# Kernel tuning notes

Hardware: AMD Instinct MI355X
Metric: run time of the kernel (lower is better)

## Reference

```python
import jax, jax.numpy as jnp
import numpy as np

SCALE = 0.125  # 1/sqrt(d_head=64)

def setup_inputs() -> dict:
    key = jax.random.key(0)
    kq, kk, kv = jax.random.split(key, 3)
    B, S, D = 16, 2048, 64
    q = jax.random.normal(kq, (B, S, D), dtype=jnp.float32)
    k = jax.random.normal(kk, (B, S, D), dtype=jnp.float32)
    v = jax.random.normal(kv, (B, S, D), dtype=jnp.float32)
    return {"q": q, "k": k, "v": v}

def reference(q, k, v):
    # scores: [B, S, S] = q @ k^T * scale
    scores = jnp.einsum('bqd,bkd->bqk', q, k) * SCALE
    attention = jax.nn.softmax(scores, axis=2)
    # dropout p=0.0 -> identity (eval); attn_mask=None -> no masking
    context = jnp.einsum('bqk,bkd->bqd', attention, v)
    return (context, attention)
```

## Files before the change

kernel.cpp:

```cpp
#include <hip/hip_runtime.h>

#define BB 16
#define SS 2048
#define DD 64
#define L2E 1.44269504f
#define A3C 4.32808512f

typedef _Float16 half8 __attribute__((ext_vector_type(8)));
typedef _Float16 half4 __attribute__((ext_vector_type(4)));
typedef float f32x4 __attribute__((ext_vector_type(4)));

typedef const __attribute__((address_space(1))) void* gas_ptr;
typedef __attribute__((address_space(3))) void* las_ptr;

#define TILE_SYNC(N)                                            \
  do {                                                          \
    asm volatile("s_waitcnt vmcnt(" #N ")" ::: "memory");       \
    __builtin_amdgcn_s_barrier();                               \
    __builtin_amdgcn_sched_barrier(0);                          \
  } while (0)

__global__ __launch_bounds__(256) void setup_kernel(const float* __restrict__ K,
                                                    const float* __restrict__ V,
                                                    _Float16* __restrict__ Kh,
                                                    _Float16* __restrict__ VT) {
  __shared__ float tile[64][65];
  int b = blockIdx.x >> 5, kt = blockIdx.x & 31;
  int tid = threadIdx.x;
  size_t base = ((size_t)b * SS + (size_t)kt * 64) * DD;
  const float4* Kq = (const float4*)(K + base);
  const float4* Vq = (const float4*)(V + base);
  half4* Khq = (half4*)(Kh + base);
#pragma unroll
  for (int it = 0; it < 4; ++it) {
    int i = tid + it * 256;
    float4 kv = Kq[i];
    half4 h;
    h[0] = (_Float16)kv.x; h[1] = (_Float16)kv.y;
    h[2] = (_Float16)kv.z; h[3] = (_Float16)kv.w;
    Khq[i] = h;
    float4 vv = Vq[i];
    int row = i >> 4, c4 = (i & 15) << 2;
    tile[row][c4 + 0] = vv.x; tile[row][c4 + 1] = vv.y;
    tile[row][c4 + 2] = vv.z; tile[row][c4 + 3] = vv.w;
  }
  __syncthreads();
  int d = tid >> 2, seg = tid & 3;
  half8 o0, o1;
#pragma unroll
  for (int j = 0; j < 8; ++j) o0[j] = (_Float16)tile[seg * 16 + j][d];
#pragma unroll
  for (int j = 0; j < 8; ++j) o1[j] = (_Float16)tile[seg * 16 + 8 + j][d];
  _Float16* dst = VT + ((size_t)b * DD + d) * SS + (size_t)kt * 64 + seg * 16;
  *(half8*)dst = o0;
  *(half8*)(dst + 8) = o1;
}

__device__ __forceinline__ void stage64(const _Float16* __restrict__ gbase, size_t rstride,
                                        _Float16* lds, int tid) {
  int w = tid >> 6, lam = tid & 63;
#pragma unroll
  for (int a = 0; a < 2; ++a) {
    int rloc = lam >> 3;
    int r = w * 16 + a * 8 + rloc;
    int byt = ((lam & 7) * 16) ^ (rloc << 4);
    const _Float16* g = gbase + (size_t)r * rstride + (byt >> 1);
    _Float16* lp = lds + (w * 16 + a * 8) * 64;
    __builtin_amdgcn_global_load_lds((gas_ptr)g, (las_ptr)lp, 16, 0, 0);
  }
}

__global__ __launch_bounds__(256, 2) void attn_kernel(const float* __restrict__ Q,
                                                      const _Float16* __restrict__ Kh,
                                                      const _Float16* __restrict__ VT,
                                                      float* __restrict__ ctx_out,
                                                      float* __restrict__ attn_out) {
  __shared__ __attribute__((aligned(16))) _Float16 Kl[2][64 * 64];
  __shared__ __attribute__((aligned(16))) _Float16 Vl[2][64 * 64];

  int tid = threadIdx.x;
  int w = tid >> 6, l = tid & 63, g = l >> 4, c = l & 15;
  int bid = (int)blockIdx.x;
  int remap = (bid & 7) * 64 + (bid >> 3);
  int b = remap >> 5, qb = remap & 31;
  size_t qrow0 = (size_t)b * SS + (size_t)qb * 64;
  size_t qr = qrow0 + (size_t)w * 16;
  const _Float16* KB = Kh + (size_t)b * SS * DD;
  const _Float16* VB = VT + (size_t)b * DD * SS;
  int swz = (c & 7) << 4;

  stage64(KB, DD, Kl[0], tid);

  half8 qa0, qa1;
  {
    const float* Qp = Q + (qr + c) * DD + 8 * g;
    float4 v0 = *(const float4*)(Qp);
    float4 v1 = *(const float4*)(Qp + 4);
    float4 v2 = *(const float4*)(Qp + 32);
    float4 v3 = *(const float4*)(Qp + 36);
    qa0[0] = (_Float16)(v0.x * 0.125f); qa0[1] = (_Float16)(v0.y * 0.125f);
    qa0[2] = (_Float16)(v0.z * 0.125f); qa0[3] = (_Float16)(v0.w * 0.125f);
    qa0[4] = (_Float16)(v1.x * 0.125f); qa0[5] = (_Float16)(v1.y * 0.125f);
    qa0[6] = (_Float16)(v1.z * 0.125f); qa0[7] = (_Float16)(v1.w * 0.125f);
    qa1[0] = (_Float16)(v2.x * 0.125f); qa1[1] = (_Float16)(v2.y * 0.125f);
    qa1[2] = (_Float16)(v2.z * 0.125f); qa1[3] = (_Float16)(v2.w * 0.125f);
    qa1[4] = (_Float16)(v3.x * 0.125f); qa1[5] = (_Float16)(v3.y * 0.125f);
    qa1[6] = (_Float16)(v3.z * 0.125f); qa1[7] = (_Float16)(v3.w * 0.125f);
  }

  TILE_SYNC(0);

  float lsum = 0.f;
  int cur = 0;
  for (int t = 0; t < 32; ++t) {
    if (t < 31) stage64(KB + (size_t)(t + 1) * 64 * DD, DD, Kl[cur ^ 1], tid);
#pragma unroll
    for (int kt = 0; kt < 4; ++kt) {
      const _Float16* kb = &Kl[cur][(kt * 16 + c) * 64];
      half8 kf0 = *(const half8*)(kb + (((16 * g) ^ swz) >> 1));
      half8 kf1 = *(const half8*)(kb + (((64 + 16 * g) ^ swz) >> 1));
      f32x4 s = {0.f, 0.f, 0.f, 0.f};
      s = __builtin_amdgcn_mfma_f32_16x16x32_f16(kf0, qa0, s, 0, 0, 0);
      s = __builtin_amdgcn_mfma_f32_16x16x32_f16(kf1, qa1, s, 0, 0, 0);
      lsum += exp2f(fmaf(s[0], L2E, -A3C)) + exp2f(fmaf(s[1], L2E, -A3C)) +
              exp2f(fmaf(s[2], L2E, -A3C)) + exp2f(fmaf(s[3], L2E, -A3C));
    }
    if (t < 31) { TILE_SYNC(0); cur ^= 1; }
  }
  lsum += __shfl_xor(lsum, 16);
  lsum += __shfl_xor(lsum, 32);
  float Ac = -__log2f(lsum) - A3C;

  __syncthreads();

  stage64(KB, DD, Kl[0], tid);
  stage64(VB, SS, Vl[0], tid);
  TILE_SYNC(0);

  f32x4 cacc[4] = {{0.f, 0.f, 0.f, 0.f}, {0.f, 0.f, 0.f, 0.f},
                   {0.f, 0.f, 0.f, 0.f}, {0.f, 0.f, 0.f, 0.f}};
  cur = 0;
  for (int t = 0; t < 32; ++t) {
    if (t < 31) {
      stage64(KB + (size_t)(t + 1) * 64 * DD, DD, Kl[cur ^ 1], tid);
      stage64(VB + (size_t)(t + 1) * 64, SS, Vl[cur ^ 1], tid);
    }
#pragma unroll
    for (int kt = 0; kt < 4; ++kt) {
      const _Float16* kb = &Kl[cur][(kt * 16 + c) * 64];
      half8 kf0 = *(const half8*)(kb + (((16 * g) ^ swz) >> 1));
      half8 kf1 = *(const half8*)(kb + (((64 + 16 * g) ^ swz) >> 1));
      f32x4 s = {0.f, 0.f, 0.f, 0.f};
      s = __builtin_amdgcn_mfma_f32_16x16x32_f16(kf0, qa0, s, 0, 0, 0);
      s = __builtin_amdgcn_mfma_f32_16x16x32_f16(kf1, qa1, s, 0, 0, 0);

      float p0 = exp2f(fmaf(s[0], L2E, Ac));
      float p1 = exp2f(fmaf(s[1], L2E, Ac));
      float p2 = exp2f(fmaf(s[2], L2E, Ac));
      float p3 = exp2f(fmaf(s[3], L2E, Ac));
      float4 st = {p0, p1, p2, p3};
      *(float4*)(attn_out + (qr + c) * SS + t * 64 + kt * 16 + 4 * g) = st;

      half4 pf;
      pf[0] = (_Float16)p0; pf[1] = (_Float16)p1;
      pf[2] = (_Float16)p2; pf[3] = (_Float16)p3;
#pragma unroll
      for (int dt = 0; dt < 4; ++dt) {
        const _Float16* vb = &Vl[cur][(dt * 16 + c) * 64];
        half4 vf = *(const half4*)(vb + (((32 * kt + 8 * g) ^ swz) >> 1));
        cacc[dt] = __builtin_amdgcn_mfma_f32_16x16x16f16(pf, vf, cacc[dt], 0, 0, 0);
      }
    }
    if (t < 31) { TILE_SYNC(4); cur ^= 1; }
  }

#pragma unroll
  for (int dt = 0; dt < 4; ++dt)
#pragma unroll
    for (int j = 0; j < 4; ++j)
      ctx_out[(qr + 4 * g + j) * DD + dt * 16 + c] = cacc[dt][j];
}

extern "C" void kernel_launch(void* const* d_in, const int* in_sizes, int n_in,
                              void* d_out, int out_size, void* d_ws, size_t ws_size,
                              hipStream_t stream) {
  const float* q = (const float*)d_in[0];
  const float* k = (const float*)d_in[1];
  const float* v = (const float*)d_in[2];
  float* ctx = (float*)d_out;
  float* attn = ctx + (size_t)BB * SS * DD;
  _Float16* Kh = (_Float16*)d_ws;
  _Float16* VT = Kh + (size_t)BB * SS * DD;
  setup_kernel<<<dim3(BB * 32), dim3(256), 0, stream>>>(k, v, Kh, VT);
  attn_kernel<<<dim3(BB * 32), dim3(256), 0, stream>>>(q, Kh, VT, ctx, attn);
}
```

Measured before the change: 103.2 us.

## Split softmax-denominator pass into its own kernel and drop LDS staging

Moves the row-sum (log-sum-exp) pass into a separate sumk kernel that splits keys across four waves, writes a per-row offset to workspace, and uses many more blocks. The main attention kernel now reads K and V^T fragments straight from global memory instead of double-buffered LDS staging with barriers. Each 16-row query slab is split across two waves by key halves, with partial contexts reduced through shared memory. The aim is more parallelism and occupancy and no per-tile barriers, at the cost of an extra launch and possibly less efficient, uncoalesced direct global fragment loads.

```diff
diff --git a/kernel.cpp b/kernel.cpp
--- a/kernel.cpp
+++ b/kernel.cpp
@@ -9,16 +9,6 @@
 typedef _Float16 half8 __attribute__((ext_vector_type(8)));
 typedef _Float16 half4 __attribute__((ext_vector_type(4)));
 typedef float f32x4 __attribute__((ext_vector_type(4)));
-
-typedef const __attribute__((address_space(1))) void* gas_ptr;
-typedef __attribute__((address_space(3))) void* las_ptr;
-
-#define TILE_SYNC(N)                                            \
-  do {                                                          \
-    asm volatile("s_waitcnt vmcnt(" #N ")" ::: "memory");       \
-    __builtin_amdgcn_s_barrier();                               \
-    __builtin_amdgcn_sched_barrier(0);                          \
-  } while (0)
 
 __global__ __launch_bounds__(256) void setup_kernel(const float* __restrict__ K,
                                                     const float* __restrict__ V,
@@ -56,129 +46,133 @@
   *(half8*)(dst + 8) = o1;
 }
 
-__device__ __forceinline__ void stage64(const _Float16* __restrict__ gbase, size_t rstride,
-                                        _Float16* lds, int tid) {
-  int w = tid >> 6, lam = tid & 63;
-#pragma unroll
-  for (int a = 0; a < 2; ++a) {
-    int rloc = lam >> 3;
-    int r = w * 16 + a * 8 + rloc;
-    int byt = ((lam & 7) * 16) ^ (rloc << 4);
-    const _Float16* g = gbase + (size_t)r * rstride + (byt >> 1);
-    _Float16* lp = lds + (w * 16 + a * 8) * 64;
-    __builtin_amdgcn_global_load_lds((gas_ptr)g, (las_ptr)lp, 16, 0, 0);
+__device__ __forceinline__ void load_qfrag(const float* __restrict__ Qp,
+                                           half8& qa0, half8& qa1) {
+  float4 v0 = *(const float4*)(Qp);
+  float4 v1 = *(const float4*)(Qp + 4);
+  float4 v2 = *(const float4*)(Qp + 32);
+  float4 v3 = *(const float4*)(Qp + 36);
+  qa0[0] = (_Float16)(v0.x * 0.125f); qa0[1] = (_Float16)(v0.y * 0.125f);
+  qa0[2] = (_Float16)(v0.z * 0.125f); qa0[3] = (_Float16)(v0.w * 0.125f);
+  qa0[4] = (_Float16)(v1.x * 0.125f); qa0[5] = (_Float16)(v1.y * 0.125f);
+  qa0[6] = (_Float16)(v1.z * 0.125f); qa0[7] = (_Float16)(v1.w * 0.125f);
+  qa1[0] = (_Float16)(v2.x * 0.125f); qa1[1] = (_Float16)(v2.y * 0.125f);
+  qa1[2] = (_Float16)(v2.z * 0.125f); qa1[3] = (_Float16)(v2.w * 0.125f);
+  qa1[4] = (_Float16)(v3.x * 0.125f); qa1[5] = (_Float16)(v3.y * 0.125f);
+  qa1[6] = (_Float16)(v3.z * 0.125f); qa1[7] = (_Float16)(v3.w * 0.125f);
+}
+
+__global__ __launch_bounds__(256, 8) void sumk_kernel(const float* __restrict__ Q,
+                                                      const _Float16* __restrict__ Kh,
+                                                      float* __restrict__ Ac) {
+  __shared__ float red[4][16];
+  int tid = threadIdx.x;
+  int w = tid >> 6, l = tid & 63, g = l >> 4, c = l & 15;
+  int bid = (int)blockIdx.x;
+  int remap = (bid & 7) * 256 + (bid >> 3);
+  int b = remap >> 7, qb = remap & 127;
+  size_t qr = (size_t)b * SS + (size_t)qb * 16;
+
+  half8 qa0, qa1;
+  load_qfrag(Q + (qr + c) * DD + 8 * g, qa0, qa1);
+
+  const _Float16* KhB = Kh + ((size_t)b * SS + w * 512 + c) * DD + 8 * g;
+  float lsum = 0.f;
+#pragma unroll 4
+  for (int t = 0; t < 32; ++t) {
+    const _Float16* kr = KhB + (size_t)t * 16 * DD;
+    half8 kf0 = *(const half8*)(kr);
+    half8 kf1 = *(const half8*)(kr + 32);
+    f32x4 s = {0.f, 0.f, 0.f, 0.f};
+    s = __builtin_amdgcn_mfma_f32_16x16x32_f16(kf0, qa0, s, 0, 0, 0);
+    s = __builtin_amdgcn_mfma_f32_16x16x32_f16(kf1, qa1, s, 0, 0, 0);
+    lsum += exp2f(fmaf(s[0], L2E, -A3C)) + exp2f(fmaf(s[1], L2E, -A3C)) +
+            exp2f(fmaf(s[2], L2E, -A3C)) + exp2f(fmaf(s[3], L2E, -A3C));
+  }
+  lsum += __shfl_xor(lsum, 16);
+  lsum += __shfl_xor(lsum, 32);
+  if (l < 16) red[w][l] = lsum;
+  __syncthreads();
+  if (tid < 16) {
+    float total = red[0][tid] + red[1][tid] + red[2][tid] + red[3][tid];
+    Ac[qr + tid] = -__log2f(total) - A3C;
   }
 }
 
-__global__ __launch_bounds__(256, 2) void attn_kernel(const float* __restrict__ Q,
+__global__ __launch_bounds__(256, 4) void attn_kernel(const float* __restrict__ Q,
                                                       const _Float16* __restrict__ Kh,
                                                       const _Float16* __restrict__ VT,
+                                                      const float* __restrict__ Ac,
                                                       float* __restrict__ ctx_out,
                                                       float* __restrict__ attn_out) {
-  __shared__ __attribute__((aligned(16))) _Float16 Kl[2][64 * 64];
-  __shared__ __attribute__((aligned(16))) _Float16 Vl[2][64 * 64];
+  __shared__ float cb[2][16][68];
 
   int tid = threadIdx.x;
   int w = tid >> 6, l = tid & 63, g = l >> 4, c = l & 15;
   int bid = (int)blockIdx.x;
-  int remap = (bid & 7) * 64 + (bid >> 3);
-  int b = remap >> 5, qb = remap & 31;
-  size_t qrow0 = (size_t)b * SS + (size_t)qb * 64;
-  size_t qr = qrow0 + (size_t)w * 16;
-  const _Float16* KB = Kh + (size_t)b * SS * DD;
-  const _Float16* VB = VT + (size_t)b * DD * SS;
-  int swz = (c & 7) << 4;
-
-  stage64(KB, DD, Kl[0], tid);
+  int remap = (bid & 7) * 128 + (bid >> 3);
+  int b = remap >> 6, qb = remap & 63;
+  size_t qr = (size_t)b * SS + (size_t)qb * 32 + (size_t)(w >> 1) * 16;
+  int k0 = (w & 1) << 10;
 
   half8 qa0, qa1;
-  {
-    const float* Qp = Q + (qr + c) * DD + 8 * g;
-    float4 v0 = *(const float4*)(Qp);
-    float4 v1 = *(const float4*)(Qp + 4);
-    float4 v2 = *(const float4*)(Qp + 32);
-    float4 v3 = *(const float4*)(Qp + 36);
-    qa0[0] = (_Float16)(v0.x * 0.125f); qa0[1] = (_Float16)(v0.y * 0.125f);
-    qa0[2] = (_Float16)(v0.z * 0.125f); qa0[3] = (_Float16)(v0.w * 0.125f);
-    qa0[4] = (_Float16)(v1.x * 0.125f); qa0[5] = (_Float16)(v1.y * 0.125f);
-    qa0[6] = (_Float16)(v1.z * 0.125f); qa0[7] = (_Float16)(v1.w * 0.125f);
-    qa1[0] = (_Float16)(v2.x * 0.125f); qa1[1] = (_Float16)(v2.y * 0.125f);
-    qa1[2] = (_Float16)(v2.z * 0.125f); qa1[3] = (_Float16)(v2.w * 0.125f);
-    qa1[4] = (_Float16)(v3.x * 0.125f); qa1[5] = (_Float16)(v3.y * 0.125f);
-    qa1[6] = (_Float16)(v3.z * 0.125f); qa1[7] = (_Float16)(v3.w * 0.125f);
-  }
+  load_qfrag(Q + (qr + c) * DD + 8 * g, qa0, qa1);
+  float ac = Ac[qr + c];
 
-  TILE_SYNC(0);
-
-  float lsum = 0.f;
-  int cur = 0;
-  for (int t = 0; t < 32; ++t) {
-    if (t < 31) stage64(KB + (size_t)(t + 1) * 64 * DD, DD, Kl[cur ^ 1], tid);
-#pragma unroll
-    for (int kt = 0; kt < 4; ++kt) {
-      const _Float16* kb = &Kl[cur][(kt * 16 + c) * 64];
-      half8 kf0 = *(const half8*)(kb + (((16 * g) ^ swz) >> 1));
-      half8 kf1 = *(const half8*)(kb + (((64 + 16 * g) ^ swz) >> 1));
-      f32x4 s = {0.f, 0.f, 0.f, 0.f};
-      s = __builtin_amdgcn_mfma_f32_16x16x32_f16(kf0, qa0, s, 0, 0, 0);
-      s = __builtin_amdgcn_mfma_f32_16x16x32_f16(kf1, qa1, s, 0, 0, 0);
-      lsum += exp2f(fmaf(s[0], L2E, -A3C)) + exp2f(fmaf(s[1], L2E, -A3C)) +
-              exp2f(fmaf(s[2], L2E, -A3C)) + exp2f(fmaf(s[3], L2E, -A3C));
-    }
-    if (t < 31) { TILE_SYNC(0); cur ^= 1; }
-  }
-  lsum += __shfl_xor(lsum, 16);
-  lsum += __shfl_xor(lsum, 32);
-  float Ac = -__log2f(lsum) - A3C;
-
-  __syncthreads();
-
-  stage64(KB, DD, Kl[0], tid);
-  stage64(VB, SS, Vl[0], tid);
-  TILE_SYNC(0);
+  const _Float16* KhB = Kh + ((size_t)b * SS + k0 + c) * DD + 8 * g;
+  const _Float16* VTB = VT + ((size_t)b * DD + c) * SS + k0 + 4 * g;
+  float* ap0 = attn_out + (qr + c) * SS + k0 + 4 * g;
 
   f32x4 cacc[4] = {{0.f, 0.f, 0.f, 0.f}, {0.f, 0.f, 0.f, 0.f},
                    {0.f, 0.f, 0.f, 0.f}, {0.f, 0.f, 0.f, 0.f}};
-  cur = 0;
-  for (int t = 0; t < 32; ++t) {
-    if (t < 31) {
-      stage64(KB + (size_t)(t + 1) * 64 * DD, DD, Kl[cur ^ 1], tid);
-      stage64(VB + (size_t)(t + 1) * 64, SS, Vl[cur ^ 1], tid);
-    }
-#pragma unroll
-    for (int kt = 0; kt < 4; ++kt) {
-      const _Float16* kb = &Kl[cur][(kt * 16 + c) * 64];
-      half8 kf0 = *(const half8*)(kb + (((16 * g) ^ swz) >> 1));
-      half8 kf1 = *(const half8*)(kb + (((64 + 16 * g) ^ swz) >> 1));
-      f32x4 s = {0.f, 0.f, 0.f, 0.f};
-      s = __builtin_amdgcn_mfma_f32_16x16x32_f16(kf0, qa0, s, 0, 0, 0);
-      s = __builtin_amdgcn_mfma_f32_16x16x32_f16(kf1, qa1, s, 0, 0, 0);
 
-      float p0 = exp2f(fmaf(s[0], L2E, Ac));
-      float p1 = exp2f(fmaf(s[1], L2E, Ac));
-      float p2 = exp2f(fmaf(s[2], L2E, Ac));
-      float p3 = exp2f(fmaf(s[3], L2E, Ac));
-      float4 st = {p0, p1, p2, p3};
-      *(float4*)(attn_out + (qr + c) * SS + t * 64 + kt * 16 + 4 * g) = st;
+#pragma unroll 2
+  for (int t = 0; t < 64; ++t) {
+    const _Float16* kr = KhB + (size_t)t * 16 * DD;
+    half8 kf0 = *(const half8*)(kr);
+    half8 kf1 = *(const half8*)(kr + 32);
+    half4 vf0 = *(const half4*)(VTB + t * 16);
+    half4 vf1 = *(const half4*)(VTB + 16 * SS + t * 16);
+    half4 vf2 = *(const half4*)(VTB + 32 * SS + t * 16);
+    half4 vf3 = *(const half4*)(VTB + 48 * SS + t * 16);
 
-      half4 pf;
-      pf[0] = (_Float16)p0; pf[1] = (_Float16)p1;
-      pf[2] = (_Float16)p2; pf[3] = (_Float16)p3;
-#pragma unroll
-      for (int dt = 0; dt < 4; ++dt) {
-        const _Float16* vb = &Vl[cur][(dt * 16 + c) * 64];
-        half4 vf = *(const half4*)(vb + (((32 * kt + 8 * g) ^ swz) >> 1));
-        cacc[dt] = __builtin_amdgcn_mfma_f32_16x16x16f16(pf, vf, cacc[dt], 0, 0, 0);
-      }
-    }
-    if (t < 31) { TILE_SYNC(4); cur ^= 1; }
+    f32x4 s = {0.f, 0.f, 0.f, 0.f};
+    s = __builtin_amdgcn_mfma_f32_16x16x32_f16(kf0, qa0, s, 0, 0, 0);
+    s = __builtin_amdgcn_mfma_f32_16x16x32_f16(kf1, qa1, s, 0, 0, 0);
+
+    float p0 = exp2f(fmaf(s[0], L2E, ac));
+    float p1 = exp2f(fmaf(s[1], L2E, ac));
+    float p2 = exp2f(fmaf(s[2], L2E, ac));
+    float p3 = exp2f(fmaf(s[3], L2E, ac));
+    float4 st = {p0, p1, p2, p3};
+    *(float4*)(ap0 + t * 16) = st;
+
+    half4 pf;
+    pf[0] = (_Float16)p0; pf[1] = (_Float16)p1;
+    pf[2] = (_Float16)p2; pf[3] = (_Float16)p3;
+    cacc[0] = __builtin_amdgcn_mfma_f32_16x16x16f16(pf, vf0, cacc[0], 0, 0, 0);
+    cacc[1] = __builtin_amdgcn_mfma_f32_16x16x16f16(pf, vf1, cacc[1], 0, 0, 0);
+    cacc[2] = __builtin_amdgcn_mfma_f32_16x16x16f16(pf, vf2, cacc[2], 0, 0, 0);
+    cacc[3] = __builtin_amdgcn_mfma_f32_16x16x16f16(pf, vf3, cacc[3], 0, 0, 0);
   }
 
+  int pair = w >> 1;
+  if (w & 1) {
 #pragma unroll
-  for (int dt = 0; dt < 4; ++dt)
+    for (int dt = 0; dt < 4; ++dt)
 #pragma unroll
-    for (int j = 0; j < 4; ++j)
-      ctx_out[(qr + 4 * g + j) * DD + dt * 16 + c] = cacc[dt][j];
+      for (int j = 0; j < 4; ++j)
+        cb[pair][4 * g + j][dt * 16 + c] = cacc[dt][j];
+  }
+  __syncthreads();
+  if (!(w & 1)) {
+#pragma unroll
+    for (int dt = 0; dt < 4; ++dt)
+#pragma unroll
+      for (int j = 0; j < 4; ++j)
+        ctx_out[(qr + 4 * g + j) * DD + dt * 16 + c] =
+            cacc[dt][j] + cb[pair][4 * g + j][dt * 16 + c];
+  }
 }
 
 extern "C" void kernel_launch(void* const* d_in, const int* in_sizes, int n_in,
@@ -191,6 +185,8 @@
   float* attn = ctx + (size_t)BB * SS * DD;
   _Float16* Kh = (_Float16*)d_ws;
   _Float16* VT = Kh + (size_t)BB * SS * DD;
+  float* Ac = (float*)(VT + (size_t)BB * DD * SS);
   setup_kernel<<<dim3(BB * 32), dim3(256), 0, stream>>>(k, v, Kh, VT);
-  attn_kernel<<<dim3(BB * 32), dim3(256), 0, stream>>>(q, Kh, VT, ctx, attn);
+  sumk_kernel<<<dim3(BB * 128), dim3(256), 0, stream>>>(q, Kh, Ac);
+  attn_kernel<<<dim3(BB * 64), dim3(256), 0, stream>>>(q, Kh, VT, Ac, ctx, attn);
 }
```

Result: slower. 257.8 us (+149.9%).

## Split softmax normalizer pass into a separate kernel launch

Applied to the files above, without the earlier changes.

Moves the first pass, which computes the row-wise log-sum-exp over all keys, into its own sumk_kernel that writes per-row constants to workspace. The attention kernel then reloads Q and the constant and runs only the normalize-store-PV pass. This lets the normalizer pass run without the Vl LDS allocation, and lets the two phases be scheduled as separate grids, possibly improving occupancy or overlap. The cost is an extra launch, reloading Q, and the Ac buffer round trip through memory.

```diff
diff --git a/kernel.cpp b/kernel.cpp
--- a/kernel.cpp
+++ b/kernel.cpp
@@ -70,43 +70,39 @@
   }
 }
 
-__global__ __launch_bounds__(256, 2) void attn_kernel(const float* __restrict__ Q,
+__device__ __forceinline__ void load_qfrag(const float* __restrict__ Qp,
+                                           half8& qa0, half8& qa1) {
+  float4 v0 = *(const float4*)(Qp);
+  float4 v1 = *(const float4*)(Qp + 4);
+  float4 v2 = *(const float4*)(Qp + 32);
+  float4 v3 = *(const float4*)(Qp + 36);
+  qa0[0] = (_Float16)(v0.x * 0.125f); qa0[1] = (_Float16)(v0.y * 0.125f);
+  qa0[2] = (_Float16)(v0.z * 0.125f); qa0[3] = (_Float16)(v0.w * 0.125f);
+  qa0[4] = (_Float16)(v1.x * 0.125f); qa0[5] = (_Float16)(v1.y * 0.125f);
+  qa0[6] = (_Float16)(v1.z * 0.125f); qa0[7] = (_Float16)(v1.w * 0.125f);
+  qa1[0] = (_Float16)(v2.x * 0.125f); qa1[1] = (_Float16)(v2.y * 0.125f);
+  qa1[2] = (_Float16)(v2.z * 0.125f); qa1[3] = (_Float16)(v2.w * 0.125f);
+  qa1[4] = (_Float16)(v3.x * 0.125f); qa1[5] = (_Float16)(v3.y * 0.125f);
+  qa1[6] = (_Float16)(v3.z * 0.125f); qa1[7] = (_Float16)(v3.w * 0.125f);
+}
+
+__global__ __launch_bounds__(256, 2) void sumk_kernel(const float* __restrict__ Q,
                                                       const _Float16* __restrict__ Kh,
-                                                      const _Float16* __restrict__ VT,
-                                                      float* __restrict__ ctx_out,
-                                                      float* __restrict__ attn_out) {
+                                                      float* __restrict__ Ac) {
   __shared__ __attribute__((aligned(16))) _Float16 Kl[2][64 * 64];
-  __shared__ __attribute__((aligned(16))) _Float16 Vl[2][64 * 64];
-
   int tid = threadIdx.x;
   int w = tid >> 6, l = tid & 63, g = l >> 4, c = l & 15;
   int bid = (int)blockIdx.x;
   int remap = (bid & 7) * 64 + (bid >> 3);
   int b = remap >> 5, qb = remap & 31;
-  size_t qrow0 = (size_t)b * SS + (size_t)qb * 64;
-  size_t qr = qrow0 + (size_t)w * 16;
+  size_t qr = (size_t)b * SS + (size_t)qb * 64 + (size_t)w * 16;
   const _Float16* KB = Kh + (size_t)b * SS * DD;
-  const _Float16* VB = VT + (size_t)b * DD * SS;
   int swz = (c & 7) << 4;
 
   stage64(KB, DD, Kl[0], tid);
 
   half8 qa0, qa1;
-  {
-    const float* Qp = Q + (qr + c) * DD + 8 * g;
-    float4 v0 = *(const float4*)(Qp);
-    float4 v1 = *(const float4*)(Qp + 4);
-    float4 v2 = *(const float4*)(Qp + 32);
-    float4 v3 = *(const float4*)(Qp + 36);
-    qa0[0] = (_Float16)(v0.x * 0.125f); qa0[1] = (_Float16)(v0.y * 0.125f);
-    qa0[2] = (_Float16)(v0.z * 0.125f); qa0[3] = (_Float16)(v0.w * 0.125f);
-    qa0[4] = (_Float16)(v1.x * 0.125f); qa0[5] = (_Float16)(v1.y * 0.125f);
-    qa0[6] = (_Float16)(v1.z * 0.125f); qa0[7] = (_Float16)(v1.w * 0.125f);
-    qa1[0] = (_Float16)(v2.x * 0.125f); qa1[1] = (_Float16)(v2.y * 0.125f);
-    qa1[2] = (_Float16)(v2.z * 0.125f); qa1[3] = (_Float16)(v2.w * 0.125f);
-    qa1[4] = (_Float16)(v3.x * 0.125f); qa1[5] = (_Float16)(v3.y * 0.125f);
-    qa1[6] = (_Float16)(v3.z * 0.125f); qa1[7] = (_Float16)(v3.w * 0.125f);
-  }
+  load_qfrag(Q + (qr + c) * DD + 8 * g, qa0, qa1);
 
   TILE_SYNC(0);
 
@@ -129,17 +125,40 @@
   }
   lsum += __shfl_xor(lsum, 16);
   lsum += __shfl_xor(lsum, 32);
-  float Ac = -__log2f(lsum) - A3C;
-
-  __syncthreads();
+  if (l < 16) Ac[qr + l] = -__log2f(lsum) - A3C;
+}
+
+__global__ __launch_bounds__(256, 2) void attn_kernel(const float* __restrict__ Q,
+                                                      const _Float16* __restrict__ Kh,
+                                                      const _Float16* __restrict__ VT,
+                                                      const float* __restrict__ Ac,
+                                                      float* __restrict__ ctx_out,
+                                                      float* __restrict__ attn_out) {
+  __shared__ __attribute__((aligned(16))) _Float16 Kl[2][64 * 64];
+  __shared__ __attribute__((aligned(16))) _Float16 Vl[2][64 * 64];
+
+  int tid = threadIdx.x;
+  int w = tid >> 6, l = tid & 63, g = l >> 4, c = l & 15;
+  int bid = (int)blockIdx.x;
+  int remap = (bid & 7) * 64 + (bid >> 3);
+  int b = remap >> 5, qb = remap & 31;
+  size_t qr = (size_t)b * SS + (size_t)qb * 64 + (size_t)w * 16;
+  const _Float16* KB = Kh + (size_t)b * SS * DD;
+  const _Float16* VB = VT + (size_t)b * DD * SS;
+  int swz = (c & 7) << 4;
 
   stage64(KB, DD, Kl[0], tid);
   stage64(VB, SS, Vl[0], tid);
+
+  half8 qa0, qa1;
+  load_qfrag(Q + (qr + c) * DD + 8 * g, qa0, qa1);
+  float ac = Ac[qr + c];
+
   TILE_SYNC(0);
 
   f32x4 cacc[4] = {{0.f, 0.f, 0.f, 0.f}, {0.f, 0.f, 0.f, 0.f},
                    {0.f, 0.f, 0.f, 0.f}, {0.f, 0.f, 0.f, 0.f}};
-  cur = 0;
+  int cur = 0;
   for (int t = 0; t < 32; ++t) {
     if (t < 31) {
       stage64(KB + (size_t)(t + 1) * 64 * DD, DD, Kl[cur ^ 1], tid);
@@ -154,10 +173,10 @@
       s = __builtin_amdgcn_mfma_f32_16x16x32_f16(kf0, qa0, s, 0, 0, 0);
       s = __builtin_amdgcn_mfma_f32_16x16x32_f16(kf1, qa1, s, 0, 0, 0);
 
-      float p0 = exp2f(fmaf(s[0], L2E, Ac));
-      float p1 = exp2f(fmaf(s[1], L2E, Ac));
-      float p2 = exp2f(fmaf(s[2], L2E, Ac));
-      float p3 = exp2f(fmaf(s[3], L2E, Ac));
+      float p0 = exp2f(fmaf(s[0], L2E, ac));
+      float p1 = exp2f(fmaf(s[1], L2E, ac));
+      float p2 = exp2f(fmaf(s[2], L2E, ac));
+      float p3 = exp2f(fmaf(s[3], L2E, ac));
       float4 st = {p0, p1, p2, p3};
       *(float4*)(attn_out + (qr + c) * SS + t * 64 + kt * 16 + 4 * g) = st;
 
@@ -191,6 +210,8 @@
   float* attn = ctx + (size_t)BB * SS * DD;
   _Float16* Kh = (_Float16*)d_ws;
   _Float16* VT = Kh + (size_t)BB * SS * DD;
+  float* Ac = (float*)(VT + (size_t)BB * DD * SS);
   setup_kernel<<<dim3(BB * 32), dim3(256), 0, stream>>>(k, v, Kh, VT);
-  attn_kernel<<<dim3(BB * 32), dim3(256), 0, stream>>>(q, Kh, VT, ctx, attn);
-}
+  sumk_kernel<<<dim3(BB * 32), dim3(256), 0, stream>>>(q, Kh, Ac);
+  attn_kernel<<<dim3(BB * 32), dim3(256), 0, stream>>>(q, Kh, VT, Ac, ctx, attn);
+}
```

Result: slower. 113.6 us (+10.1%).

## Triple-buffer K/V LDS tiles with prefetch distance two and single barrier

Applied to the files above, without the earlier changes.

Grows the K and V shared-memory staging from two buffers to three and prefetches tiles two iterations ahead. Each loop iteration now uses one barrier at the top, with vmcnt counts chosen so that one tile of async global->LDS loads stays in flight while the current tile is computed. This targets the load latency exposed in both passes over K/V, which are bandwidth-heavy because of the large attention-matrix stores. In exchange, shared memory per block rises to 48KB, which could limit occupancy, and the hand-computed vmcnt values are fragile because the attention stores also count against vmcnt.

```diff
diff --git a/kernel.cpp b/kernel.cpp
--- a/kernel.cpp
+++ b/kernel.cpp
@@ -70,53 +70,54 @@
   }
 }
 
+__device__ __forceinline__ void load_qfrag(const float* __restrict__ Qp,
+                                           half8& qa0, half8& qa1) {
+  float4 v0 = *(const float4*)(Qp);
+  float4 v1 = *(const float4*)(Qp + 4);
+  float4 v2 = *(const float4*)(Qp + 32);
+  float4 v3 = *(const float4*)(Qp + 36);
+  qa0[0] = (_Float16)(v0.x * 0.125f); qa0[1] = (_Float16)(v0.y * 0.125f);
+  qa0[2] = (_Float16)(v0.z * 0.125f); qa0[3] = (_Float16)(v0.w * 0.125f);
+  qa0[4] = (_Float16)(v1.x * 0.125f); qa0[5] = (_Float16)(v1.y * 0.125f);
+  qa0[6] = (_Float16)(v1.z * 0.125f); qa0[7] = (_Float16)(v1.w * 0.125f);
+  qa1[0] = (_Float16)(v2.x * 0.125f); qa1[1] = (_Float16)(v2.y * 0.125f);
+  qa1[2] = (_Float16)(v2.z * 0.125f); qa1[3] = (_Float16)(v2.w * 0.125f);
+  qa1[4] = (_Float16)(v3.x * 0.125f); qa1[5] = (_Float16)(v3.y * 0.125f);
+  qa1[6] = (_Float16)(v3.z * 0.125f); qa1[7] = (_Float16)(v3.w * 0.125f);
+}
+
 __global__ __launch_bounds__(256, 2) void attn_kernel(const float* __restrict__ Q,
                                                       const _Float16* __restrict__ Kh,
                                                       const _Float16* __restrict__ VT,
                                                       float* __restrict__ ctx_out,
                                                       float* __restrict__ attn_out) {
-  __shared__ __attribute__((aligned(16))) _Float16 Kl[2][64 * 64];
-  __shared__ __attribute__((aligned(16))) _Float16 Vl[2][64 * 64];
+  __shared__ __attribute__((aligned(16))) _Float16 Kl[3][64 * 64];
+  __shared__ __attribute__((aligned(16))) _Float16 Vl[3][64 * 64];
 
   int tid = threadIdx.x;
   int w = tid >> 6, l = tid & 63, g = l >> 4, c = l & 15;
   int bid = (int)blockIdx.x;
   int remap = (bid & 7) * 64 + (bid >> 3);
   int b = remap >> 5, qb = remap & 31;
-  size_t qrow0 = (size_t)b * SS + (size_t)qb * 64;
-  size_t qr = qrow0 + (size_t)w * 16;
+  size_t qr = (size_t)b * SS + (size_t)qb * 64 + (size_t)w * 16;
   const _Float16* KB = Kh + (size_t)b * SS * DD;
   const _Float16* VB = VT + (size_t)b * DD * SS;
   int swz = (c & 7) << 4;
 
   stage64(KB, DD, Kl[0], tid);
+  stage64(KB + (size_t)64 * DD, DD, Kl[1], tid);
 
   half8 qa0, qa1;
-  {
-    const float* Qp = Q + (qr + c) * DD + 8 * g;
-    float4 v0 = *(const float4*)(Qp);
-    float4 v1 = *(const float4*)(Qp + 4);
-    float4 v2 = *(const float4*)(Qp + 32);
-    float4 v3 = *(const float4*)(Qp + 36);
-    qa0[0] = (_Float16)(v0.x * 0.125f); qa0[1] = (_Float16)(v0.y * 0.125f);
-    qa0[2] = (_Float16)(v0.z * 0.125f); qa0[3] = (_Float16)(v0.w * 0.125f);
-    qa0[4] = (_Float16)(v1.x * 0.125f); qa0[5] = (_Float16)(v1.y * 0.125f);
-    qa0[6] = (_Float16)(v1.z * 0.125f); qa0[7] = (_Float16)(v1.w * 0.125f);
-    qa1[0] = (_Float16)(v2.x * 0.125f); qa1[1] = (_Float16)(v2.y * 0.125f);
-    qa1[2] = (_Float16)(v2.z * 0.125f); qa1[3] = (_Float16)(v2.w * 0.125f);
-    qa1[4] = (_Float16)(v3.x * 0.125f); qa1[5] = (_Float16)(v3.y * 0.125f);
-    qa1[6] = (_Float16)(v3.z * 0.125f); qa1[7] = (_Float16)(v3.w * 0.125f);
-  }
-
-  TILE_SYNC(0);
+  load_qfrag(Q + (qr + c) * DD + 8 * g, qa0, qa1);
 
   float lsum = 0.f;
-  int cur = 0;
+  int bufc = 0, bufs = 2;
   for (int t = 0; t < 32; ++t) {
-    if (t < 31) stage64(KB + (size_t)(t + 1) * 64 * DD, DD, Kl[cur ^ 1], tid);
+    if (t < 31) TILE_SYNC(2); else TILE_SYNC(0);
+    if (t + 2 < 32) stage64(KB + (size_t)(t + 2) * 64 * DD, DD, Kl[bufs], tid);
 #pragma unroll
     for (int kt = 0; kt < 4; ++kt) {
-      const _Float16* kb = &Kl[cur][(kt * 16 + c) * 64];
+      const _Float16* kb = &Kl[bufc][(kt * 16 + c) * 64];
       half8 kf0 = *(const half8*)(kb + (((16 * g) ^ swz) >> 1));
       half8 kf1 = *(const half8*)(kb + (((64 + 16 * g) ^ swz) >> 1));
       f32x4 s = {0.f, 0.f, 0.f, 0.f};
@@ -125,39 +126,45 @@
       lsum += exp2f(fmaf(s[0], L2E, -A3C)) + exp2f(fmaf(s[1], L2E, -A3C)) +
               exp2f(fmaf(s[2], L2E, -A3C)) + exp2f(fmaf(s[3], L2E, -A3C));
     }
-    if (t < 31) { TILE_SYNC(0); cur ^= 1; }
+    bufc = (bufc == 2) ? 0 : bufc + 1;
+    bufs = (bufs == 2) ? 0 : bufs + 1;
   }
   lsum += __shfl_xor(lsum, 16);
   lsum += __shfl_xor(lsum, 32);
-  float Ac = -__log2f(lsum) - A3C;
+  float ac = -__log2f(lsum) - A3C;
 
   __syncthreads();
 
   stage64(KB, DD, Kl[0], tid);
   stage64(VB, SS, Vl[0], tid);
-  TILE_SYNC(0);
+  stage64(KB + (size_t)64 * DD, DD, Kl[1], tid);
+  stage64(VB + 64, SS, Vl[1], tid);
 
   f32x4 cacc[4] = {{0.f, 0.f, 0.f, 0.f}, {0.f, 0.f, 0.f, 0.f},
                    {0.f, 0.f, 0.f, 0.f}, {0.f, 0.f, 0.f, 0.f}};
-  cur = 0;
+  bufc = 0; bufs = 2;
   for (int t = 0; t < 32; ++t) {
-    if (t < 31) {
-      stage64(KB + (size_t)(t + 1) * 64 * DD, DD, Kl[cur ^ 1], tid);
-      stage64(VB + (size_t)(t + 1) * 64, SS, Vl[cur ^ 1], tid);
+    if (t == 0) TILE_SYNC(4);
+    else if (t == 1) TILE_SYNC(8);
+    else if (t < 31) TILE_SYNC(12);
+    else TILE_SYNC(8);
+    if (t + 2 < 32) {
+      stage64(KB + (size_t)(t + 2) * 64 * DD, DD, Kl[bufs], tid);
+      stage64(VB + (size_t)(t + 2) * 64, SS, Vl[bufs], tid);
     }
 #pragma unroll
     for (int kt = 0; kt < 4; ++kt) {
-      const _Float16* kb = &Kl[cur][(kt * 16 + c) * 64];
+      const _Float16* kb = &Kl[bufc][(kt * 16 + c) * 64];
       half8 kf0 = *(const half8*)(kb + (((16 * g) ^ swz) >> 1));
       half8 kf1 = *(const half8*)(kb + (((64 + 16 * g) ^ swz) >> 1));
       f32x4 s = {0.f, 0.f, 0.f, 0.f};
       s = __builtin_amdgcn_mfma_f32_16x16x32_f16(kf0, qa0, s, 0, 0, 0);
       s = __builtin_amdgcn_mfma_f32_16x16x32_f16(kf1, qa1, s, 0, 0, 0);
 
-      float p0 = exp2f(fmaf(s[0], L2E, Ac));
-      float p1 = exp2f(fmaf(s[1], L2E, Ac));
-      float p2 = exp2f(fmaf(s[2], L2E, Ac));
-      float p3 = exp2f(fmaf(s[3], L2E, Ac));
+      float p0 = exp2f(fmaf(s[0], L2E, ac));
+      float p1 = exp2f(fmaf(s[1], L2E, ac));
+      float p2 = exp2f(fmaf(s[2], L2E, ac));
+      float p3 = exp2f(fmaf(s[3], L2E, ac));
       float4 st = {p0, p1, p2, p3};
       *(float4*)(attn_out + (qr + c) * SS + t * 64 + kt * 16 + 4 * g) = st;
 
@@ -166,12 +173,13 @@
       pf[2] = (_Float16)p2; pf[3] = (_Float16)p3;
 #pragma unroll
       for (int dt = 0; dt < 4; ++dt) {
-        const _Float16* vb = &Vl[cur][(dt * 16 + c) * 64];
+        const _Float16* vb = &Vl[bufc][(dt * 16 + c) * 64];
         half4 vf = *(const half4*)(vb + (((32 * kt + 8 * g) ^ swz) >> 1));
         cacc[dt] = __builtin_amdgcn_mfma_f32_16x16x16f16(pf, vf, cacc[dt], 0, 0, 0);
       }
     }
-    if (t < 31) { TILE_SYNC(4); cur ^= 1; }
+    bufc = (bufc == 2) ? 0 : bufc + 1;
+    bufs = (bufs == 2) ? 0 : bufs + 1;
   }
 
 #pragma unroll
```

After: 95.65 us. 1.08x faster.
